# Optimization experiments

Measured on AMD Instinct MI355X. Metric: run time of the kernel, lower is better.

The kernel has to match this reference:

```python
import jax, jax.numpy as jnp
import numpy as np

N_WORDS = 30000
EMB_DIM = 784  # 28*28
MAT_DIM = 28
BATCH = 1024
SEQ_LEN = 64


def setup_inputs() -> dict:
    key = jax.random.key(0)
    k_sent, k_tab = jax.random.split(key)
    # token ids in [0, n_words]; row 0 is the neutral (identity) / padding element
    sent = jax.random.randint(k_sent, (BATCH, SEQ_LEN), 0, N_WORDS + 1, dtype=jnp.int32).astype(jnp.int64)
    eye_flat = jnp.eye(MAT_DIM, dtype=jnp.float32).reshape(-1)
    # 'identity' init strategy: identity + small gaussian noise (scale kept small for stability of long products)
    table = eye_flat + 0.01 * jax.random.normal(k_tab, (N_WORDS + 1, EMB_DIM), dtype=jnp.float32)
    table = table.at[0].set(eye_flat)  # neutral element at padding_idx=0
    return {"sent": sent, "table": table}


def reference(sent, table):
    # sent: [B, S] int ids; table: [n_words+1, d*d]
    B, S = sent.shape
    d = MAT_DIM
    word_mats = table[sent].reshape(B, S, d, d)  # embedding lookup + unflatten
    # CMOW: continual multiplication cur = cur @ W_i, sequential over seq dim
    init = word_mats[:, 0]                      # [B, d, d]
    rest = jnp.moveaxis(word_mats[:, 1:], 1, 0)  # [S-1, B, d, d]

    def step(cur, w):
        return jnp.matmul(cur, w), None

    cur, _ = jax.lax.scan(step, init, rest)
    return cur.reshape(B, d * d)  # flatten matrix back to embedding
```

## Files before the change

kernel.cpp:

```cpp
#include <hip/hip_runtime.h>
#include <stdint.h>

#define SEQ 64
#define D 28
#define EMB 784
#define CH 8
#define BUFF 832
#define BUFW 1024
#define CTW 36
#define CTSZ (32 * CTW)

typedef float float4v __attribute__((ext_vector_type(4)));
typedef __bf16 bf16x8 __attribute__((ext_vector_type(8)));

union FragU { unsigned u[4]; bf16x8 v; };

__device__ __forceinline__ unsigned fbits(float x) { union { float f; unsigned u; } t; t.f = x; return t.u; }
__device__ __forceinline__ float fof(unsigned u) { union { unsigned u; float f; } t; t.u = u; return t.f; }

__device__ __forceinline__ void split_frags(const float x[8], bf16x8& hi, bf16x8& lo)
{
    FragU H, L;
#pragma unroll
    for (int p = 0; p < 4; ++p) {
        unsigned ua = fbits(x[2 * p]), ub = fbits(x[2 * p + 1]);
        H.u[p] = (ua >> 16) | (ub & 0xFFFF0000u);
        unsigned la = fbits(x[2 * p]     - fof(ua & 0xFFFF0000u));
        unsigned lb = fbits(x[2 * p + 1] - fof(ub & 0xFFFF0000u));
        L.u[p] = (la >> 16) | (lb & 0xFFFF0000u);
    }
    hi = H.v; lo = L.v;
}

__device__ __forceinline__ void dma_row(const float* grow, float* lbuf, int lane)
{
    const char* g16 = (const char*)grow + lane * 16;
    const char* g4  = (const char*)grow + 3072 + lane * 4;
    char* l = (char*)lbuf;
    __builtin_amdgcn_global_load_lds((const __attribute__((address_space(1))) void*)(g16),
                                     (__attribute__((address_space(3))) void*)(l), 16, 0, 0);
    __builtin_amdgcn_global_load_lds((const __attribute__((address_space(1))) void*)(g16 + 1024),
                                     (__attribute__((address_space(3))) void*)(l + 1024), 16, 0, 0);
    __builtin_amdgcn_global_load_lds((const __attribute__((address_space(1))) void*)(g16 + 2048),
                                     (__attribute__((address_space(3))) void*)(l + 2048), 16, 0, 0);
    __builtin_amdgcn_global_load_lds((const __attribute__((address_space(1))) void*)(g4),
                                     (__attribute__((address_space(3))) void*)(l + 3072), 4, 0, 0);
}

__global__ __launch_bounds__(256, 1) void w2m_leaf_mfma(
    const int* __restrict__ sent,
    const float* __restrict__ table,
    float* __restrict__ ws0)
{
    __shared__ float CT[4 * CTSZ] __attribute__((aligned(16)));
    __shared__ float BB[4 * 2 * BUFW] __attribute__((aligned(16)));
    const int lane = threadIdx.x & 63;
    const int wid  = threadIdx.x >> 6;
    const int w = blockIdx.x * 4 + wid;
    const int b = w >> 3;
    const int g = w & 7;
    const int c = lane & 15;
    const int quad = lane >> 4;
    const bool q3 = (quad == 3);
    float* CTw = &CT[wid * CTSZ];
    float* B0 = &BB[wid * 2 * BUFW];
    float* B1 = B0 + BUFW;

    const int myidx = sent[b * SEQ + 8 * g + (lane & 7)];
    int jl[CH];
#pragma unroll
    for (int j = 0; j < CH; ++j) jl[j] = __builtin_amdgcn_readlane(myidx, j);

    dma_row(table + (size_t)jl[0] * EMB, B0, lane);
    dma_row(table + (size_t)jl[1] * EMB, B1, lane);
    __builtin_amdgcn_s_waitcnt(0x0074);

    float4v acc[2][2];
#pragma unroll
    for (int R = 0; R < 2; ++R)
#pragma unroll
        for (int Cc = 0; Cc < 2; ++Cc)
#pragma unroll
            for (int i = 0; i < 4; ++i)
                acc[R][Cc][i] = B0[(16 * R + 4 * quad + i) * D + 16 * Cc + c];
    __builtin_amdgcn_s_waitcnt(0xC07F);

#pragma unroll 1
    for (int j = 1; j < CH; ++j) {
        const int jn = (j + 1 < CH) ? (j + 1) : j;
        float* nB = (j & 1) ? B0 : B1;
        float* cB = (j & 1) ? B1 : B0;
        dma_row(table + (size_t)jl[jn] * EMB, nB, lane);

#pragma unroll
        for (int R = 0; R < 2; ++R)
#pragma unroll
            for (int Cc = 0; Cc < 2; ++Cc)
#pragma unroll
                for (int i = 0; i < 4; ++i)
                    CTw[(16 * R + 4 * quad + i) * CTW + 16 * Cc + c] = acc[R][Cc][i];

        __builtin_amdgcn_sched_barrier(0);
        __builtin_amdgcn_s_waitcnt(0x0074);
        __builtin_amdgcn_sched_barrier(0);

        bf16x8 Ah[2], Al[2];
#pragma unroll
        for (int R = 0; R < 2; ++R) {
            const float* ap = CTw + (16 * R + c) * CTW + 8 * quad;
            float4v x0 = *(const float4v*)ap;
            float4v x1 = *(const float4v*)(ap + 4);
            if (q3) x1 = float4v{0.f, 0.f, 0.f, 0.f};
            float x[8] = {x0.x, x0.y, x0.z, x0.w, x1.x, x1.y, x1.z, x1.w};
            split_frags(x, Ah[R], Al[R]);
        }

        bf16x8 Bh[2], Bl[2];
#pragma unroll
        for (int Cc = 0; Cc < 2; ++Cc) {
            const float* bp = cB + (8 * quad) * D + 16 * Cc + c;
            float x[8];
#pragma unroll
            for (int t = 0; t < 8; ++t) x[t] = bp[t * D];
            if (q3) { x[4] = 0.f; x[5] = 0.f; x[6] = 0.f; x[7] = 0.f; }
            split_frags(x, Bh[Cc], Bl[Cc]);
        }

#pragma unroll
        for (int R = 0; R < 2; ++R)
#pragma unroll
            for (int Cc = 0; Cc < 2; ++Cc) {
                float4v d = {0.f, 0.f, 0.f, 0.f};
                d = __builtin_amdgcn_mfma_f32_16x16x32_bf16(Ah[R], Bh[Cc], d, 0, 0, 0);
                d = __builtin_amdgcn_mfma_f32_16x16x32_bf16(Ah[R], Bl[Cc], d, 0, 0, 0);
                d = __builtin_amdgcn_mfma_f32_16x16x32_bf16(Al[R], Bh[Cc], d, 0, 0, 0);
                acc[R][Cc] = d;
            }
    }

    float* orow = ws0 + (size_t)w * EMB;
#pragma unroll
    for (int R = 0; R < 2; ++R)
#pragma unroll
        for (int Cc = 0; Cc < 2; ++Cc)
#pragma unroll
            for (int i = 0; i < 4; ++i) {
                const int row = 16 * R + 4 * quad + i;
                const int col = 16 * Cc + c;
                if (row < D && col < D) orow[row * D + col] = acc[R][Cc][i];
            }
}

__device__ __forceinline__ void xpose_write(const float4v ct[4],
                                            float* __restrict__ LTw,
                                            int it, int jt)
{
#pragma unroll
    for (int cc = 0; cc < 4; ++cc) {
        float4v t;
        t.x = ct[0][cc]; t.y = ct[1][cc]; t.z = ct[2][cc]; t.w = ct[3][cc];
        *(float4v*)&LTw[(4 * jt + cc) * D + 4 * it] = t;
    }
}

template <int CNT, typename F>
__device__ __forceinline__ void mat_chain(F rowptr, float* __restrict__ LTw,
                                          float* __restrict__ B0,
                                          float* __restrict__ B1,
                                          float4v ct[4], int it, int jt, int lane)
{
    dma_row(rowptr(1), B1, lane);

#pragma unroll 1
    for (int j = 1; j < CNT; ++j) {
        const int jn = (j + 1 < CNT) ? (j + 1) : j;
        float* nB = (j & 1) ? B0 : B1;
        float* cB = (j & 1) ? B1 : B0;
        dma_row(rowptr(jn), nB, lane);

        xpose_write(ct, LTw, it, jt);

        __builtin_amdgcn_sched_barrier(0);
        __builtin_amdgcn_s_waitcnt(0x0074);
        __builtin_amdgcn_sched_barrier(0);

        const float* ap = LTw + 4 * it;
        const float* bp = cB + 4 * jt;
        float4v acc[4] = {};
#pragma unroll
        for (int k = 0; k < 28; ++k) {
            float4v av = *(const float4v*)(ap + k * D);
            float4v bb = *(const float4v*)(bp + k * D);
#pragma unroll
            for (int r = 0; r < 4; ++r) acc[r] += bb * av[r];
        }
#pragma unroll
        for (int r = 0; r < 4; ++r) ct[r] = acc[r];
    }
}

__global__ __launch_bounds__(64, 1) void w2m_top(
    const float* __restrict__ ws0,
    float* __restrict__ out)
{
    __shared__ float LT[EMB] __attribute__((aligned(16)));
    __shared__ float BBt[2 * BUFF] __attribute__((aligned(16)));
    const int lane = threadIdx.x;
    const int b = blockIdx.x;
    int it = lane / 7, jt = lane % 7;
    const bool act = lane < 49;
    if (!act) { it = 6; jt = 6; }

    const float* base = ws0 + (size_t)b * CH * EMB;
    float4v ct[4];
#pragma unroll
    for (int r = 0; r < 4; ++r)
        ct[r] = *(const float4v*)(base + (4 * it + r) * D + 4 * jt);

    mat_chain<CH>([&](int j) { return base + (size_t)j * EMB; },
                  LT, &BBt[0], &BBt[BUFF], ct, it, jt, lane);

    if (act) {
        float* orow = out + (size_t)b * EMB;
#pragma unroll
        for (int r = 0; r < 4; ++r)
            *(float4v*)(orow + (4 * it + r) * D + 4 * jt) = ct[r];
    }
}

__global__ __launch_bounds__(64, 1) void w2m_serial(
    const int* __restrict__ sent,
    const float* __restrict__ table,
    float* __restrict__ out)
{
    __shared__ float LT[EMB] __attribute__((aligned(16)));
    __shared__ float BBs[2 * BUFF] __attribute__((aligned(16)));
    const int lane = threadIdx.x;
    const int b = blockIdx.x;
    int it = lane / 7, jt = lane % 7;
    const bool act = lane < 49;
    if (!act) { it = 6; jt = 6; }

    const int myidx = sent[b * SEQ + lane];
    int jls[SEQ];
#pragma unroll
    for (int s = 0; s < SEQ; ++s) jls[s] = __builtin_amdgcn_readlane(myidx, s);

    const float* row0 = table + (size_t)jls[0] * EMB;
    float4v ct[4];
#pragma unroll
    for (int r = 0; r < 4; ++r)
        ct[r] = *(const float4v*)(row0 + (4 * it + r) * D + 4 * jt);

    mat_chain<SEQ>([&](int s) { return table + (size_t)jls[s] * EMB; },
                   LT, &BBs[0], &BBs[BUFF], ct, it, jt, lane);

    if (act) {
        float* orow = out + (size_t)b * EMB;
#pragma unroll
        for (int r = 0; r < 4; ++r)
            *(float4v*)(orow + (4 * it + r) * D + 4 * jt) = ct[r];
    }
}

extern "C" void kernel_launch(void* const* d_in, const int* in_sizes, int n_in,
                              void* d_out, int out_size, void* d_ws, size_t ws_size,
                              hipStream_t stream) {
    const int* sent = (const int*)d_in[0];
    const float* table = (const float*)d_in[1];
    float* out = (float*)d_out;
    const int batch = in_sizes[0] / SEQ;
    const size_t ws_needed = (size_t)batch * CH * EMB * sizeof(float);

    if (ws_size >= ws_needed) {
        float* ws0 = (float*)d_ws;
        const int waves1 = batch * CH;
        hipLaunchKernelGGL(w2m_leaf_mfma, dim3(waves1 / 4), dim3(256), 0, stream,
                           sent, table, ws0);
        hipLaunchKernelGGL(w2m_top, dim3(batch), dim3(64), 0, stream,
                           ws0, out);
    } else {
        hipLaunchKernelGGL(w2m_serial, dim3(batch), dim3(64), 0, stream,
                           sent, table, out);
    }
}
```

Before: 169.7 us.

## Use split-bf16 MFMA chain for top-level reduction and shrink leaf blocks

The top-level stage, which multiplies the 8 partial products per sentence, now uses the same split-bf16 MFMA chain as the leaf stage instead of scalar FP32 FMAs. The MFMA chain is factored into a shared template. Leaf blocks go from 4 waves to 2 with smaller LDS buffers, and top blocks now hold 2 sentences each. The initial accumulator load clamps padded indices so out-of-range lanes read valid LDS. The intent is to cut the top kernel's latency-bound scalar matmul time. The trade-off is split-bf16 (hi/lo) precision instead of full FP32 for the top stage.

```diff
diff --git a/kernel.cpp b/kernel.cpp
--- a/kernel.cpp
+++ b/kernel.cpp
@@ -6,7 +6,6 @@
 #define EMB 784
 #define CH 8
 #define BUFF 832
-#define BUFW 1024
 #define CTW 36
 #define CTSZ (32 * CTW)
 
@@ -47,50 +46,40 @@
                                      (__attribute__((address_space(3))) void*)(l + 3072), 4, 0, 0);
 }
 
-__global__ __launch_bounds__(256, 1) void w2m_leaf_mfma(
-    const int* __restrict__ sent,
-    const float* __restrict__ table,
-    float* __restrict__ ws0)
-{
-    __shared__ float CT[4 * CTSZ] __attribute__((aligned(16)));
-    __shared__ float BB[4 * 2 * BUFW] __attribute__((aligned(16)));
-    const int lane = threadIdx.x & 63;
-    const int wid  = threadIdx.x >> 6;
-    const int w = blockIdx.x * 4 + wid;
-    const int b = w >> 3;
-    const int g = w & 7;
+template <int CNT, typename F>
+__device__ __forceinline__ void mfma_chain(F rowptr,
+                                           float* __restrict__ CTw,
+                                           float* __restrict__ B0,
+                                           float* __restrict__ B1,
+                                           float4v acc[2][2],
+                                           int lane)
+{
     const int c = lane & 15;
     const int quad = lane >> 4;
     const bool q3 = (quad == 3);
-    float* CTw = &CT[wid * CTSZ];
-    float* B0 = &BB[wid * 2 * BUFW];
-    float* B1 = B0 + BUFW;
-
-    const int myidx = sent[b * SEQ + 8 * g + (lane & 7)];
-    int jl[CH];
-#pragma unroll
-    for (int j = 0; j < CH; ++j) jl[j] = __builtin_amdgcn_readlane(myidx, j);
-
-    dma_row(table + (size_t)jl[0] * EMB, B0, lane);
-    dma_row(table + (size_t)jl[1] * EMB, B1, lane);
+
+    dma_row(rowptr(0), B0, lane);
+    dma_row(rowptr(1), B1, lane);
     __builtin_amdgcn_s_waitcnt(0x0074);
 
-    float4v acc[2][2];
 #pragma unroll
     for (int R = 0; R < 2; ++R)
 #pragma unroll
         for (int Cc = 0; Cc < 2; ++Cc)
 #pragma unroll
-            for (int i = 0; i < 4; ++i)
-                acc[R][Cc][i] = B0[(16 * R + 4 * quad + i) * D + 16 * Cc + c];
+            for (int i = 0; i < 4; ++i) {
+                const int rr = 16 * R + 4 * quad + i;
+                const int cc = 16 * Cc + c;
+                acc[R][Cc][i] = B0[(rr < D ? rr : D - 1) * D + (cc < D ? cc : D - 1)];
+            }
     __builtin_amdgcn_s_waitcnt(0xC07F);
 
 #pragma unroll 1
-    for (int j = 1; j < CH; ++j) {
-        const int jn = (j + 1 < CH) ? (j + 1) : j;
+    for (int j = 1; j < CNT; ++j) {
+        const int jn = (j + 1 < CNT) ? (j + 1) : j;
         float* nB = (j & 1) ? B0 : B1;
         float* cB = (j & 1) ? B1 : B0;
-        dma_row(table + (size_t)jl[jn] * EMB, nB, lane);
+        dma_row(rowptr(jn), nB, lane);
 
 #pragma unroll
         for (int R = 0; R < 2; ++R)
@@ -137,8 +126,13 @@
                 acc[R][Cc] = d;
             }
     }
-
-    float* orow = ws0 + (size_t)w * EMB;
+}
+
+__device__ __forceinline__ void store_acc(const float4v acc[2][2],
+                                          float* __restrict__ orow, int lane)
+{
+    const int c = lane & 15;
+    const int quad = lane >> 4;
 #pragma unroll
     for (int R = 0; R < 2; ++R)
 #pragma unroll
@@ -151,6 +145,55 @@
             }
 }
 
+__global__ __launch_bounds__(128, 1) void w2m_leaf_mfma(
+    const int* __restrict__ sent,
+    const float* __restrict__ table,
+    float* __restrict__ ws0)
+{
+    __shared__ float CT[2 * CTSZ] __attribute__((aligned(16)));
+    __shared__ float BB[2 * 2 * BUFF] __attribute__((aligned(16)));
+    const int lane = threadIdx.x & 63;
+    const int wid  = threadIdx.x >> 6;
+    const int w = blockIdx.x * 2 + wid;
+    const int b = w >> 3;
+    const int g = w & 7;
+    float* CTw = &CT[wid * CTSZ];
+    float* B0 = &BB[wid * 2 * BUFF];
+    float* B1 = B0 + BUFF;
+
+    const int myidx = sent[b * SEQ + 8 * g + (lane & 7)];
+    int jl[CH];
+#pragma unroll
+    for (int j = 0; j < CH; ++j) jl[j] = __builtin_amdgcn_readlane(myidx, j);
+
+    float4v acc[2][2];
+    mfma_chain<CH>([&](int j) { return table + (size_t)jl[j] * EMB; },
+                   CTw, B0, B1, acc, lane);
+
+    store_acc(acc, ws0 + (size_t)w * EMB, lane);
+}
+
+__global__ __launch_bounds__(128, 1) void w2m_top_mfma(
+    const float* __restrict__ ws0,
+    float* __restrict__ out)
+{
+    __shared__ float CT[2 * CTSZ] __attribute__((aligned(16)));
+    __shared__ float BB[2 * 2 * BUFF] __attribute__((aligned(16)));
+    const int lane = threadIdx.x & 63;
+    const int wid  = threadIdx.x >> 6;
+    const int b = blockIdx.x * 2 + wid;
+    float* CTw = &CT[wid * CTSZ];
+    float* B0 = &BB[wid * 2 * BUFF];
+    float* B1 = B0 + BUFF;
+
+    const float* base = ws0 + (size_t)b * CH * EMB;
+    float4v acc[2][2];
+    mfma_chain<CH>([&](int j) { return base + (size_t)j * EMB; },
+                   CTw, B0, B1, acc, lane);
+
+    store_acc(acc, out + (size_t)b * EMB, lane);
+}
+
 __device__ __forceinline__ void xpose_write(const float4v ct[4],
                                             float* __restrict__ LTw,
                                             int it, int jt)
@@ -160,71 +203,6 @@
         float4v t;
         t.x = ct[0][cc]; t.y = ct[1][cc]; t.z = ct[2][cc]; t.w = ct[3][cc];
         *(float4v*)&LTw[(4 * jt + cc) * D + 4 * it] = t;
-    }
-}
-
-template <int CNT, typename F>
-__device__ __forceinline__ void mat_chain(F rowptr, float* __restrict__ LTw,
-                                          float* __restrict__ B0,
-                                          float* __restrict__ B1,
-                                          float4v ct[4], int it, int jt, int lane)
-{
-    dma_row(rowptr(1), B1, lane);
-
-#pragma unroll 1
-    for (int j = 1; j < CNT; ++j) {
-        const int jn = (j + 1 < CNT) ? (j + 1) : j;
-        float* nB = (j & 1) ? B0 : B1;
-        float* cB = (j & 1) ? B1 : B0;
-        dma_row(rowptr(jn), nB, lane);
-
-        xpose_write(ct, LTw, it, jt);
-
-        __builtin_amdgcn_sched_barrier(0);
-        __builtin_amdgcn_s_waitcnt(0x0074);
-        __builtin_amdgcn_sched_barrier(0);
-
-        const float* ap = LTw + 4 * it;
-        const float* bp = cB + 4 * jt;
-        float4v acc[4] = {};
-#pragma unroll
-        for (int k = 0; k < 28; ++k) {
-            float4v av = *(const float4v*)(ap + k * D);
-            float4v bb = *(const float4v*)(bp + k * D);
-#pragma unroll
-            for (int r = 0; r < 4; ++r) acc[r] += bb * av[r];
-        }
-#pragma unroll
-        for (int r = 0; r < 4; ++r) ct[r] = acc[r];
-    }
-}
-
-__global__ __launch_bounds__(64, 1) void w2m_top(
-    const float* __restrict__ ws0,
-    float* __restrict__ out)
-{
-    __shared__ float LT[EMB] __attribute__((aligned(16)));
-    __shared__ float BBt[2 * BUFF] __attribute__((aligned(16)));
-    const int lane = threadIdx.x;
-    const int b = blockIdx.x;
-    int it = lane / 7, jt = lane % 7;
-    const bool act = lane < 49;
-    if (!act) { it = 6; jt = 6; }
-
-    const float* base = ws0 + (size_t)b * CH * EMB;
-    float4v ct[4];
-#pragma unroll
-    for (int r = 0; r < 4; ++r)
-        ct[r] = *(const float4v*)(base + (4 * it + r) * D + 4 * jt);
-
-    mat_chain<CH>([&](int j) { return base + (size_t)j * EMB; },
-                  LT, &BBt[0], &BBt[BUFF], ct, it, jt, lane);
-
-    if (act) {
-        float* orow = out + (size_t)b * EMB;
-#pragma unroll
-        for (int r = 0; r < 4; ++r)
-            *(float4v*)(orow + (4 * it + r) * D + 4 * jt) = ct[r];
     }
 }
 
@@ -252,8 +230,36 @@
     for (int r = 0; r < 4; ++r)
         ct[r] = *(const float4v*)(row0 + (4 * it + r) * D + 4 * jt);
 
-    mat_chain<SEQ>([&](int s) { return table + (size_t)jls[s] * EMB; },
-                   LT, &BBs[0], &BBs[BUFF], ct, it, jt, lane);
+    float* Bs0 = &BBs[0];
+    float* Bs1 = &BBs[BUFF];
+    dma_row(table + (size_t)jls[1] * EMB, Bs1, lane);
+
+#pragma unroll 1
+    for (int j = 1; j < SEQ; ++j) {
+        const int jn = (j + 1 < SEQ) ? (j + 1) : j;
+        float* nB = (j & 1) ? Bs0 : Bs1;
+        float* cB = (j & 1) ? Bs1 : Bs0;
+        dma_row(table + (size_t)jls[jn] * EMB, nB, lane);
+
+        xpose_write(ct, LT, it, jt);
+
+        __builtin_amdgcn_sched_barrier(0);
+        __builtin_amdgcn_s_waitcnt(0x0074);
+        __builtin_amdgcn_sched_barrier(0);
+
+        const float* ap = LT + 4 * it;
+        const float* bp = cB + 4 * jt;
+        float4v acc[4] = {};
+#pragma unroll
+        for (int k = 0; k < 28; ++k) {
+            float4v av = *(const float4v*)(ap + k * D);
+            float4v bb = *(const float4v*)(bp + k * D);
+#pragma unroll
+            for (int r = 0; r < 4; ++r) acc[r] += bb * av[r];
+        }
+#pragma unroll
+        for (int r = 0; r < 4; ++r) ct[r] = acc[r];
+    }
 
     if (act) {
         float* orow = out + (size_t)b * EMB;
@@ -275,9 +281,9 @@
     if (ws_size >= ws_needed) {
         float* ws0 = (float*)d_ws;
         const int waves1 = batch * CH;
-        hipLaunchKernelGGL(w2m_leaf_mfma, dim3(waves1 / 4), dim3(256), 0, stream,
+        hipLaunchKernelGGL(w2m_leaf_mfma, dim3(waves1 / 2), dim3(128), 0, stream,
                            sent, table, ws0);
-        hipLaunchKernelGGL(w2m_top, dim3(batch), dim3(64), 0, stream,
+        hipLaunchKernelGGL(w2m_top_mfma, dim3(batch / 2), dim3(128), 0, stream,
                            ws0, out);
     } else {
         hipLaunchKernelGGL(w2m_serial, dim3(batch), dim3(64), 0, stream,
```

Result: faster. 163.6 us (-3.6%).
